# Performance work log

Hardware: AMD Instinct MI355X
Metric: run time of the kernel (lower is better)

The kernel has to match this reference:

```python
import jax, jax.numpy as jnp
import numpy as np

H = 256  # hidden_size
C = 512  # in_channels


def _gru_dir(x, w_ih, w_hh, b_ih, b_hh, reverse):
    # x: (B, T, Cin); w_ih: (3H, Cin); w_hh: (3H, H); gate order r,z,n (PyTorch)
    if reverse:
        x = x[:, ::-1, :]
    xp = jnp.einsum('btc,gc->btg', x, w_ih) + b_ih  # (B, T, 3H), batched GEMM
    h0 = jnp.zeros((x.shape[0], w_hh.shape[1]), x.dtype)

    def step(h, xp_t):  # xp_t: (B, 3H)
        gh = h @ w_hh.T + b_hh
        xr, xz, xn = jnp.split(xp_t, 3, axis=-1)
        hr, hz, hn = jnp.split(gh, 3, axis=-1)
        r = jax.nn.sigmoid(xr + hr)
        z = jax.nn.sigmoid(xz + hz)
        n = jnp.tanh(xn + r * hn)
        h_new = (1.0 - z) * n + z * h
        return h_new, h_new

    _, ys = jax.lax.scan(step, h0, jnp.swapaxes(xp, 0, 1))  # (T, B, H)
    ys = jnp.swapaxes(ys, 0, 1)  # (B, T, H)
    if reverse:
        ys = ys[:, ::-1, :]
    return ys


def _bigru_layer(x, wf, whf, bf, bhf, wr, whr, br, bhr):
    fwd = _gru_dir(x, wf, whf, bf, bhf, reverse=False)
    bwd = _gru_dir(x, wr, whr, br, bhr, reverse=True)
    return jnp.concatenate([fwd, bwd], axis=-1)  # (B, T, 2H)


def setup_inputs() -> dict:
    key = jax.random.key(0)
    ks = jax.random.split(key, 17)
    k = 1.0 / np.sqrt(H)  # PyTorch default init bound
    u = lambda kk, shp: jax.random.uniform(kk, shp, jnp.float32, -k, k)
    x = jax.random.normal(ks[0], (64, 512, 512, 1), jnp.float32)
    inp = {'x': x}
    # layer 0: input size C; layer 1: input size 2H
    sizes = {'l0': C, 'l1': 2 * H}
    i = 1
    for layer in ('l0', 'l1'):
        cin = sizes[layer]
        for d in ('f', 'r'):
            inp[f'w_ih_{layer}{d}'] = u(ks[i], (3 * H, cin)); i += 1
            inp[f'w_hh_{layer}{d}'] = u(ks[i], (3 * H, H)); i += 1
            inp[f'b_ih_{layer}{d}'] = u(ks[i], (3 * H,)); i += 1
            inp[f'b_hh_{layer}{d}'] = u(ks[i], (3 * H,)); i += 1
    return inp


def reference(x, w_ih_l0f, w_hh_l0f, b_ih_l0f, b_hh_l0f,
              w_ih_l0r, w_hh_l0r, b_ih_l0r, b_hh_l0r,
              w_ih_l1f, w_hh_l1f, b_ih_l1f, b_hh_l1f,
              w_ih_l1r, w_hh_l1r, b_ih_l1r, b_hh_l1r):
    b, c, w, h = x.shape
    seq = x.reshape(b, c, w * h).transpose(0, 2, 1)  # (B, T, C)
    y0 = _bigru_layer(seq, w_ih_l0f, w_hh_l0f, b_ih_l0f, b_hh_l0f,
                      w_ih_l0r, w_hh_l0r, b_ih_l0r, b_hh_l0r)
    y1 = _bigru_layer(y0, w_ih_l1f, w_hh_l1f, b_ih_l1f, b_hh_l1f,
                      w_ih_l1r, w_hh_l1r, b_ih_l1r, b_hh_l1r)
    return y1  # (B, T, 2H)
```

## Files before the change

kernel.cpp:

```cpp
#include <hip/hip_runtime.h>


typedef unsigned short u16;
typedef unsigned char u8;
typedef __attribute__((ext_vector_type(8))) short short8;
typedef __attribute__((ext_vector_type(4))) float f32x4;
typedef __attribute__((ext_vector_type(4))) int i32x4;

#define C1 (-1.4426950408889634f)
#define C2 (-2.8853900817779268f)
#define QS 258064.0f
#define C1S (C1 / QS)
#define C2S (C2 / QS)
#define MAGIC 12582912.0f

static __device__ __forceinline__ u16 f2bf(float x){
  union { float f; unsigned u; } v; v.f = x;
  unsigned r = v.u + 0x7fffu + ((v.u >> 16) & 1u);
  return (u16)(r >> 16);
}
static __device__ __forceinline__ float bf2f(u16 b){
  union { float f; unsigned u; } v; v.u = ((unsigned)b) << 16;
  return v.f;
}
static __device__ __forceinline__ unsigned cvt_pk_bf16(float lo, float hi){
  unsigned d;
  asm("v_cvt_pk_bf16_f32 %0, %1, %2" : "=v"(d) : "v"(lo), "v"(hi));
  return d;
}
static __device__ __forceinline__ unsigned q8(float x, float scale){
  union { float f; unsigned u; } v; v.f = fmaf(x, scale, MAGIC);
  return v.u & 0xffu;
}
#if __has_builtin(__builtin_amdgcn_exp2f)
#define EXP2(x) __builtin_amdgcn_exp2f(x)
#else
#define EXP2(x) exp2f(x)
#endif
#define RCP(x) __builtin_amdgcn_rcpf(x)
#define MFI8(a,b,c) __builtin_amdgcn_mfma_i32_16x16x64_i8((a),(b),(c),0,0,0)

#define TT 512
#define BB 64
#define HH 256
#define GG 768
#define CC 512

#define HLB 320

__global__ __launch_bounds__(256) void k_wconv(const float* __restrict__ wf,
    const float* __restrict__ wr, u16* __restrict__ Wb)
{
  const int idx = (blockIdx.x * 256 + threadIdx.x) * 4;
  const int half = GG * CC;
  const float* src = (idx < half) ? (wf + idx) : (wr + (idx - half));
  float4 v = *(const float4*)src;
  unsigned p0 = (unsigned)f2bf(v.x) | ((unsigned)f2bf(v.y) << 16);
  unsigned p1 = (unsigned)f2bf(v.z) | ((unsigned)f2bf(v.w) << 16);
  *(uint2*)&Wb[idx] = make_uint2(p0, p1);
}

__global__ __launch_bounds__(256) void k_transpose(const float* __restrict__ x,
                                                   u16* __restrict__ xT)
{
  __shared__ u16 tile[32][33];
  const int b  = blockIdx.z;
  const int c0 = blockIdx.y * 32, t0 = blockIdx.x * 32;
  const int tx = threadIdx.x & 31, ty = threadIdx.x >> 5;
  const float* xb = x + (size_t)b * CC * TT;
  #pragma unroll
  for (int i = 0; i < 4; ++i){
    int c = c0 + ty + i * 8;
    tile[ty + i * 8][tx] = f2bf(xb[(size_t)c * TT + t0 + tx]);
  }
  __syncthreads();
  const int bb2 = b >> 1, mrow = b & 1;
  #pragma unroll
  for (int i = 0; i < 4; ++i){
    int t = t0 + ty + i * 8;
    size_t rowp = ((size_t)bb2 * TT + t) * 2 + mrow;
    xT[rowp * CC + c0 + tx] = tile[tx][ty + i * 8];
  }
}

__global__ __launch_bounds__(256) void k_gemm(const u16* __restrict__ A,
    const u16* __restrict__ Wb,
    const float* __restrict__ bif, const float* __restrict__ bir,
    const float* __restrict__ bhf, const float* __restrict__ bhr,
    u16* __restrict__ xpA, u16* __restrict__ xpB)
{
  __shared__ u16 As[64][72];
  __shared__ u16 Bs[64][72];
  const int tid = threadIdx.x;
  const int n0  = blockIdx.x * 64;
  const int m0  = blockIdx.y * 64;
  const int dir = (n0 >= GG) ? 1 : 0;
  const int gb  = n0 - dir * GG;
  const float* BI = dir ? bir : bif;
  const float* BH = dir ? bhr : bhf;

  const int w = tid >> 6, l = tid & 63, q = l >> 4, r = l & 15;
  f32x4 acc[4] = {};

  for (int k0 = 0; k0 < CC; k0 += 64){
    #pragma unroll
    for (int i = 0; i < 2; ++i){
      int ch = tid + 256 * i;
      int row = ch >> 3, c8 = ch & 7;
      *(uint4*)&As[row][c8 * 8] =
          *(const uint4*)&A[(size_t)(m0 + row) * CC + k0 + c8 * 8];
      *(uint4*)&Bs[row][c8 * 8] =
          *(const uint4*)&Wb[(size_t)(n0 + row) * CC + k0 + c8 * 8];
    }
    __syncthreads();
    #pragma unroll
    for (int kk = 0; kk < 2; ++kk){
      short8 a = *(const short8*)&As[w * 16 + r][kk * 32 + q * 8];
      #pragma unroll
      for (int nt = 0; nt < 4; ++nt){
        short8 b = *(const short8*)&Bs[nt * 16 + r][kk * 32 + q * 8];
        acc[nt] = __builtin_amdgcn_mfma_f32_16x16x32_bf16(a, b, acc[nt], 0, 0, 0);
      }
    }
    __syncthreads();
  }
  #pragma unroll
  for (int nt = 0; nt < 4; ++nt){
    const int g  = gb + nt * 16 + r;
    const int gi = g >> 8;
    const int c  = g & 255;
    const int wvl = c >> 5, cw = c & 31;
    const int ct = cw >> 4, rp = cw & 15;
    const float bias = (gi < 2) ? (BI[g] + BH[g]) : BI[g];
    const float sc   = (gi < 2) ? C1 : C2;
    #pragma unroll
    for (int j = 0; j < 4; ++j){
      const int row  = m0 + w * 16 + q * 4 + j;
      const int t    = (row >> 1) & 511;
      const int bb2  = row >> 10;
      const int mrow = row & 1;
      const int lane = wvl * 64 + (ct * 2 + mrow) * 16 + rp;
      const size_t base = ((size_t)(dir * 32 + bb2) * TT + t) * 512 + lane;
      const u16 v = f2bf(sc * (acc[nt][j] + bias));
      if (gi < 2) xpA[base * 2 + gi] = v;
      else        xpB[base]          = v;
    }
  }
}

template<int OUT_F32>
__global__ __launch_bounds__(512, 2) void k_rec(
    const u16* __restrict__ xpA, const u16* __restrict__ xpB,
    const float* __restrict__ whf, const float* __restrict__ whr,
    const float* __restrict__ bhf, const float* __restrict__ bhr,
    void* __restrict__ yout)
{
  __shared__ __align__(16) u8 hl[2][2][HLB];
  const int tid = threadIdx.x;
  const int d = blockIdx.x >> 5, bb2 = blockIdx.x & 31;
  const int wv = tid >> 6, l = tid & 63, q = l >> 4, r = l & 15;
  const int upper = (l >= 32);
  const int rodd  = q & 1;
  const int rl = l & 1;
  const float* WH = d ? whr : whf;
  const float* BH = d ? bhr : bhf;

  i32x4 Bf[3][2][4];
  #pragma unroll
  for (int gi = 0; gi < 3; ++gi)
    #pragma unroll
    for (int ct = 0; ct < 2; ++ct){
      int g = gi * HH + wv * 32 + ct * 16 + r;
      #pragma unroll
      for (int kk = 0; kk < 4; ++kk){
        const float* s = &WH[(size_t)g * HH + kk * 64 + q * 16];
        i32x4 bfv;
        #pragma unroll
        for (int c4 = 0; c4 < 4; ++c4){
          float4 fv = *(const float4*)(s + c4 * 4);
          unsigned b0 = q8(fv.x, 2032.0f);
          unsigned b1 = q8(fv.y, 2032.0f);
          unsigned b2 = q8(fv.z, 2032.0f);
          unsigned b3 = q8(fv.w, 2032.0f);
          bfv[c4] = (int)(b0 | (b1 << 8) | (b2 << 16) | (b3 << 24));
        }
        Bf[gi][ct][kk] = bfv;
      }
    }

  const int col = wv * 32 + (upper ? 16 : 0) + r;
  const float bnl = C2 * BH[2 * HH + col];
  float ho = 0.0f;
  const i32x4 ZACC = {};

  for (int i = tid; i < 2 * 2 * HLB; i += 512) ((u8*)hl)[i] = 0;

  const int t0 = d ? (TT - 1) : 0;
  const int dstep = d ? -1 : 1;

  const size_t blk = (size_t)(d * 32 + bb2) * TT;
  const u16* pxA = xpA + ((blk + t0) * 512 + tid) * 2;
  const u16* pxB = xpB + ((blk + t0) * 512 + tid);
  const ptrdiff_t pxAs = (ptrdiff_t)dstep * 512 * 2;
  const ptrdiff_t pxBs = (ptrdiff_t)dstep * 512;

  struct XP { unsigned a; u16 b; };
  XP cxA, cxB;
  cxA.a = *(const unsigned*)pxA;  cxA.b = *pxB;
  pxA += pxAs; pxB += pxBs;

  u16*   py = nullptr;  float* pf = nullptr;
  if (OUT_F32){
    float* yf = (float*)yout;
    pf = yf + (((size_t)(bb2 * 2 + rodd) * TT + t0) * (2 * HH)) + (size_t)d * HH + col;
  } else {
    u16* yb = (u16*)yout;
    py = yb + (((size_t)bb2 * TT + t0) * 2 + rodd) * 512 + (size_t)d * HH + col;
  }
  const ptrdiff_t pys = (ptrdiff_t)dstep * 2 * 512;
  const ptrdiff_t pfs = (ptrdiff_t)dstep * 2 * HH;

  __syncthreads();

  auto step = [&](int s, int cur, XP* cxu, XP* cxl) {
    const int nxt = cur ^ 1;
    cxl->a = *(const unsigned*)pxA;
    cxl->b = *pxB;
    pxA += pxAs; pxB += pxBs;

    i32x4 af0 = *(const i32x4*)&hl[cur][rl][0 * 64 + q * 16];
    i32x4 af1 = *(const i32x4*)&hl[cur][rl][1 * 64 + q * 16];
    i32x4 af2 = *(const i32x4*)&hl[cur][rl][2 * 64 + q * 16];
    i32x4 af3 = *(const i32x4*)&hl[cur][rl][3 * 64 + q * 16];

    i32x4 a00 = MFI8(af0, Bf[0][0][0], ZACC);
    i32x4 a01 = MFI8(af0, Bf[0][1][0], ZACC);
    i32x4 a10 = MFI8(af0, Bf[1][0][0], ZACC);
    i32x4 a11 = MFI8(af0, Bf[1][1][0], ZACC);
    a00 = MFI8(af1, Bf[0][0][1], a00);  a01 = MFI8(af1, Bf[0][1][1], a01);
    a10 = MFI8(af1, Bf[1][0][1], a10);  a11 = MFI8(af1, Bf[1][1][1], a11);
    a00 = MFI8(af2, Bf[0][0][2], a00);  a01 = MFI8(af2, Bf[0][1][2], a01);
    a10 = MFI8(af2, Bf[1][0][2], a10);  a11 = MFI8(af2, Bf[1][1][2], a11);
    a00 = MFI8(af3, Bf[0][0][3], a00);  a01 = MFI8(af3, Bf[0][1][3], a01);
    a10 = MFI8(af3, Bf[1][0][3], a10);  a11 = MFI8(af3, Bf[1][1][3], a11);
    i32x4 a20 = MFI8(af0, Bf[2][0][0], ZACC);
    i32x4 a21 = MFI8(af0, Bf[2][1][0], ZACC);
    a20 = MFI8(af1, Bf[2][0][1], a20);  a21 = MFI8(af1, Bf[2][1][1], a21);
    a20 = MFI8(af2, Bf[2][0][2], a20);  a21 = MFI8(af2, Bf[2][1][2], a21);
    a20 = MFI8(af3, Bf[2][0][3], a20);  a21 = MFI8(af3, Bf[2][1][3], a21);

    int e00 = upper ? a01[0] : a00[0];
    int e01 = upper ? a01[1] : a00[1];
    int e10 = upper ? a11[0] : a10[0];
    int e11 = upper ? a11[1] : a10[1];
    float a0f = (float)(rodd ? e01 : e00);
    float a1f = (float)(rodd ? e11 : e10);
    float xrp = bf2f((u16)(cxu->a & 0xffffu));
    float xzp = bf2f((u16)(cxu->a >> 16));
    float er = EXP2(fmaf(a0f, C1S, xrp));
    float ez = EXP2(fmaf(a1f, C1S, xzp));
    float sr = 1.0f + er, sz = 1.0f + ez;
    float R  = RCP(sr * sz);
    float rr = sz * R;
    float zz = sr * R;
    int e20 = upper ? a21[0] : a20[0];
    int e21 = upper ? a21[1] : a20[1];
    float a2f = (float)(rodd ? e21 : e20);
    float xnp = bf2f(cxu->b);
    float inner = fmaf(a2f, C2S, bnl);
    float e2 = EXP2(fmaf(rr, inner, xnp));
    float nn = fmaf(2.0f, RCP(1.0f + e2), -1.0f);
    float hv = fmaf(zz, ho - nn, nn);
    ho = hv;
    hl[nxt][rodd][col] = (u8)q8(hv, 127.0f);
    if (OUT_F32){
      pf[0] = hv;
      pf += pfs;
    } else {
      py[0] = (u16)cvt_pk_bf16(hv, hv);
      py += pys;
    }
    asm volatile("s_waitcnt lgkmcnt(0)" ::: "memory");
    __builtin_amdgcn_s_barrier();
    asm volatile("" ::: "memory");
  };

  #pragma unroll 1
  for (int s = 0; s < TT; s += 2){
    step(s,     0, &cxA, &cxB);
    step(s + 1, 1, &cxB, &cxA);
  }
}

extern "C" void kernel_launch(void* const* d_in, const int* in_sizes, int n_in,
                              void* d_out, int out_size, void* d_ws, size_t ws_size,
                              hipStream_t stream)
{
  const float* x        = (const float*)d_in[0];
  const float* w_ih_l0f = (const float*)d_in[1];
  const float* w_hh_l0f = (const float*)d_in[2];
  const float* b_ih_l0f = (const float*)d_in[3];
  const float* b_hh_l0f = (const float*)d_in[4];
  const float* w_ih_l0r = (const float*)d_in[5];
  const float* w_hh_l0r = (const float*)d_in[6];
  const float* b_ih_l0r = (const float*)d_in[7];
  const float* b_hh_l0r = (const float*)d_in[8];
  const float* w_ih_l1f = (const float*)d_in[9];
  const float* w_hh_l1f = (const float*)d_in[10];
  const float* b_ih_l1f = (const float*)d_in[11];
  const float* b_hh_l1f = (const float*)d_in[12];
  const float* w_ih_l1r = (const float*)d_in[13];
  const float* w_hh_l1r = (const float*)d_in[14];
  const float* b_ih_l1r = (const float*)d_in[15];
  const float* b_hh_l1r = (const float*)d_in[16];

  u16* xT  = (u16*)d_ws;
  u16* xpA = xT  + (size_t)BB * TT * CC;
  u16* xpB = xpA + (size_t)64 * TT * 512 * 2;
  u16* Wb  = xpB + (size_t)64 * TT * 512;
  u16* y0  = xT;
  (void)in_sizes; (void)n_in; (void)out_size; (void)ws_size;

  k_transpose<<<dim3(TT / 32, CC / 32, BB), 256, 0, stream>>>(x, xT);

  k_wconv<<<dim3(2 * GG * CC / 1024), 256, 0, stream>>>(w_ih_l0f, w_ih_l0r, Wb);
  k_gemm<<<dim3(2 * GG / 64, BB * TT / 64), 256, 0, stream>>>(
      xT, Wb, b_ih_l0f, b_ih_l0r, b_hh_l0f, b_hh_l0r, xpA, xpB);

  k_rec<0><<<dim3(64), 512, 0, stream>>>(xpA, xpB, w_hh_l0f, w_hh_l0r, b_hh_l0f, b_hh_l0r, (void*)y0);

  k_wconv<<<dim3(2 * GG * CC / 1024), 256, 0, stream>>>(w_ih_l1f, w_ih_l1r, Wb);
  k_gemm<<<dim3(2 * GG / 64, BB * TT / 64), 256, 0, stream>>>(
      y0, Wb, b_ih_l1f, b_ih_l1r, b_hh_l1f, b_hh_l1r, xpA, xpB);

  k_rec<1><<<dim3(64), 512, 0, stream>>>(xpA, xpB, w_hh_l1f, w_hh_l1r, b_hh_l1f, b_hh_l1r, d_out);
}
```

Before: 849.2 us.

## Interleave two independent batch chains per recurrent block to hide latency

Each recurrent block now processes two batch groups (two independent recurrence chains) instead of one, halving the grid from 64 to 32 blocks. The MFMA and gate work of the two chains is interleaved inside each timestep so one chain's latency can overlap the other's, and the two chains share a single barrier per step. The cost is twice the serial per-step work per block, more registers and shared memory, and use of only half as many CUs on a latency-bound kernel.

```diff
diff --git a/kernel.cpp b/kernel.cpp
--- a/kernel.cpp
+++ b/kernel.cpp
@@ -155,9 +155,10 @@
     const float* __restrict__ bhf, const float* __restrict__ bhr,
     void* __restrict__ yout)
 {
-  __shared__ __align__(16) u8 hl[2][2][HLB];
+  __shared__ __align__(16) u8 hl[2][2][2][HLB];
   const int tid = threadIdx.x;
-  const int d = blockIdx.x >> 5, bb2 = blockIdx.x & 31;
+  const int d  = blockIdx.x >> 4;
+  const int qd = blockIdx.x & 15;
   const int wv = tid >> 6, l = tid & 63, q = l >> 4, r = l & 15;
   const int upper = (l >= 32);
   const int rodd  = q & 1;
@@ -190,73 +191,56 @@
 
   const int col = wv * 32 + (upper ? 16 : 0) + r;
   const float bnl = C2 * BH[2 * HH + col];
-  float ho = 0.0f;
+  float hoA = 0.0f, hoB = 0.0f;
   const i32x4 ZACC = {};
 
-  for (int i = tid; i < 2 * 2 * HLB; i += 512) ((u8*)hl)[i] = 0;
+  for (int i = tid; i < 2 * 2 * 2 * HLB; i += 512) ((u8*)hl)[i] = 0;
 
   const int t0 = d ? (TT - 1) : 0;
   const int dstep = d ? -1 : 1;
 
-  const size_t blk = (size_t)(d * 32 + bb2) * TT;
-  const u16* pxA = xpA + ((blk + t0) * 512 + tid) * 2;
-  const u16* pxB = xpB + ((blk + t0) * 512 + tid);
+  const int bbA = qd * 2;
+  const size_t blkA = (size_t)(d * 32 + bbA) * TT;
+  const u16* pxAA = xpA + ((blkA + t0) * 512 + tid) * 2;
+  const u16* pxBA = xpB + ((blkA + t0) * 512 + tid);
+  const u16* pxAB = pxAA + (size_t)TT * 512 * 2;
+  const u16* pxBB = pxBA + (size_t)TT * 512;
   const ptrdiff_t pxAs = (ptrdiff_t)dstep * 512 * 2;
   const ptrdiff_t pxBs = (ptrdiff_t)dstep * 512;
 
   struct XP { unsigned a; u16 b; };
-  XP cxA, cxB;
-  cxA.a = *(const unsigned*)pxA;  cxA.b = *pxB;
-  pxA += pxAs; pxB += pxBs;
-
-  u16*   py = nullptr;  float* pf = nullptr;
+  XP cA0, cA1, cB0, cB1;
+  cA0.a = *(const unsigned*)pxAA;  cA0.b = *pxBA;
+  cB0.a = *(const unsigned*)pxAB;  cB0.b = *pxBB;
+  pxAA += pxAs; pxBA += pxBs; pxAB += pxAs; pxBB += pxBs;
+
+  u16 *pyA = nullptr, *pyB = nullptr;
+  float *pfA = nullptr, *pfB = nullptr;
   if (OUT_F32){
     float* yf = (float*)yout;
-    pf = yf + (((size_t)(bb2 * 2 + rodd) * TT + t0) * (2 * HH)) + (size_t)d * HH + col;
+    pfA = yf + (((size_t)(bbA * 2 + rodd) * TT + t0) * (2 * HH)) + (size_t)d * HH + col;
+    pfB = pfA + (size_t)2 * TT * (2 * HH);
   } else {
     u16* yb = (u16*)yout;
-    py = yb + (((size_t)bb2 * TT + t0) * 2 + rodd) * 512 + (size_t)d * HH + col;
+    pyA = yb + (((size_t)bbA * TT + t0) * 2 + rodd) * 512 + (size_t)d * HH + col;
+    pyB = pyA + (size_t)TT * 2 * 512;
   }
   const ptrdiff_t pys = (ptrdiff_t)dstep * 2 * 512;
   const ptrdiff_t pfs = (ptrdiff_t)dstep * 2 * HH;
 
   __syncthreads();
 
-  auto step = [&](int s, int cur, XP* cxu, XP* cxl) {
-    const int nxt = cur ^ 1;
-    cxl->a = *(const unsigned*)pxA;
-    cxl->b = *pxB;
-    pxA += pxAs; pxB += pxBs;
-
-    i32x4 af0 = *(const i32x4*)&hl[cur][rl][0 * 64 + q * 16];
-    i32x4 af1 = *(const i32x4*)&hl[cur][rl][1 * 64 + q * 16];
-    i32x4 af2 = *(const i32x4*)&hl[cur][rl][2 * 64 + q * 16];
-    i32x4 af3 = *(const i32x4*)&hl[cur][rl][3 * 64 + q * 16];
-
-    i32x4 a00 = MFI8(af0, Bf[0][0][0], ZACC);
-    i32x4 a01 = MFI8(af0, Bf[0][1][0], ZACC);
-    i32x4 a10 = MFI8(af0, Bf[1][0][0], ZACC);
-    i32x4 a11 = MFI8(af0, Bf[1][1][0], ZACC);
-    a00 = MFI8(af1, Bf[0][0][1], a00);  a01 = MFI8(af1, Bf[0][1][1], a01);
-    a10 = MFI8(af1, Bf[1][0][1], a10);  a11 = MFI8(af1, Bf[1][1][1], a11);
-    a00 = MFI8(af2, Bf[0][0][2], a00);  a01 = MFI8(af2, Bf[0][1][2], a01);
-    a10 = MFI8(af2, Bf[1][0][2], a10);  a11 = MFI8(af2, Bf[1][1][2], a11);
-    a00 = MFI8(af3, Bf[0][0][3], a00);  a01 = MFI8(af3, Bf[0][1][3], a01);
-    a10 = MFI8(af3, Bf[1][0][3], a10);  a11 = MFI8(af3, Bf[1][1][3], a11);
-    i32x4 a20 = MFI8(af0, Bf[2][0][0], ZACC);
-    i32x4 a21 = MFI8(af0, Bf[2][1][0], ZACC);
-    a20 = MFI8(af1, Bf[2][0][1], a20);  a21 = MFI8(af1, Bf[2][1][1], a21);
-    a20 = MFI8(af2, Bf[2][0][2], a20);  a21 = MFI8(af2, Bf[2][1][2], a21);
-    a20 = MFI8(af3, Bf[2][0][3], a20);  a21 = MFI8(af3, Bf[2][1][3], a21);
-
+  auto gates = [&](const i32x4& a00, const i32x4& a01, const i32x4& a10,
+                   const i32x4& a11, const i32x4& a20, const i32x4& a21,
+                   unsigned xa, u16 xb, float& ho) -> float {
     int e00 = upper ? a01[0] : a00[0];
     int e01 = upper ? a01[1] : a00[1];
     int e10 = upper ? a11[0] : a10[0];
     int e11 = upper ? a11[1] : a10[1];
     float a0f = (float)(rodd ? e01 : e00);
     float a1f = (float)(rodd ? e11 : e10);
-    float xrp = bf2f((u16)(cxu->a & 0xffffu));
-    float xzp = bf2f((u16)(cxu->a >> 16));
+    float xrp = bf2f((u16)(xa & 0xffffu));
+    float xzp = bf2f((u16)(xa >> 16));
     float er = EXP2(fmaf(a0f, C1S, xrp));
     float ez = EXP2(fmaf(a1f, C1S, xzp));
     float sr = 1.0f + er, sz = 1.0f + ez;
@@ -266,19 +250,58 @@
     int e20 = upper ? a21[0] : a20[0];
     int e21 = upper ? a21[1] : a20[1];
     float a2f = (float)(rodd ? e21 : e20);
-    float xnp = bf2f(cxu->b);
+    float xnp = bf2f(xb);
     float inner = fmaf(a2f, C2S, bnl);
     float e2 = EXP2(fmaf(rr, inner, xnp));
     float nn = fmaf(2.0f, RCP(1.0f + e2), -1.0f);
     float hv = fmaf(zz, ho - nn, nn);
     ho = hv;
-    hl[nxt][rodd][col] = (u8)q8(hv, 127.0f);
+    return hv;
+  };
+
+  #define CHAIN_MFMA(CH, a00,a01,a10,a11,a20,a21)                              \
+    i32x4 af0 = *(const i32x4*)&hl[CH][cur][rl][0 * 64 + q * 16];              \
+    i32x4 af1 = *(const i32x4*)&hl[CH][cur][rl][1 * 64 + q * 16];              \
+    i32x4 af2 = *(const i32x4*)&hl[CH][cur][rl][2 * 64 + q * 16];              \
+    i32x4 af3 = *(const i32x4*)&hl[CH][cur][rl][3 * 64 + q * 16];              \
+    a00 = MFI8(af0, Bf[0][0][0], ZACC);                                        \
+    a01 = MFI8(af0, Bf[0][1][0], ZACC);                                        \
+    a10 = MFI8(af0, Bf[1][0][0], ZACC);                                        \
+    a11 = MFI8(af0, Bf[1][1][0], ZACC);                                        \
+    a00 = MFI8(af1, Bf[0][0][1], a00);  a01 = MFI8(af1, Bf[0][1][1], a01);     \
+    a10 = MFI8(af1, Bf[1][0][1], a10);  a11 = MFI8(af1, Bf[1][1][1], a11);     \
+    a00 = MFI8(af2, Bf[0][0][2], a00);  a01 = MFI8(af2, Bf[0][1][2], a01);     \
+    a10 = MFI8(af2, Bf[1][0][2], a10);  a11 = MFI8(af2, Bf[1][1][2], a11);     \
+    a00 = MFI8(af3, Bf[0][0][3], a00);  a01 = MFI8(af3, Bf[0][1][3], a01);     \
+    a10 = MFI8(af3, Bf[1][0][3], a10);  a11 = MFI8(af3, Bf[1][1][3], a11);     \
+    a20 = MFI8(af0, Bf[2][0][0], ZACC);                                        \
+    a21 = MFI8(af0, Bf[2][1][0], ZACC);                                        \
+    a20 = MFI8(af1, Bf[2][0][1], a20);  a21 = MFI8(af1, Bf[2][1][1], a21);     \
+    a20 = MFI8(af2, Bf[2][0][2], a20);  a21 = MFI8(af2, Bf[2][1][2], a21);     \
+    a20 = MFI8(af3, Bf[2][0][3], a20);  a21 = MFI8(af3, Bf[2][1][3], a21);
+
+  auto step = [&](int cur, XP* cAu, XP* cAl, XP* cBu, XP* cBl) {
+    const int nxt = cur ^ 1;
+    cAl->a = *(const unsigned*)pxAA;  cAl->b = *pxBA;
+    cBl->a = *(const unsigned*)pxAB;  cBl->b = *pxBB;
+    pxAA += pxAs; pxBA += pxBs; pxAB += pxAs; pxBB += pxBs;
+
+    i32x4 A00, A01, A10, A11, A20, A21;
+    { CHAIN_MFMA(0, A00, A01, A10, A11, A20, A21) }
+    i32x4 B00, B01, B10, B11, B20, B21;
+    { CHAIN_MFMA(1, B00, B01, B10, B11, B20, B21) }
+
+    float hvA = gates(A00, A01, A10, A11, A20, A21, cAu->a, cAu->b, hoA);
+    hl[0][nxt][rodd][col] = (u8)q8(hvA, 127.0f);
+    float hvB = gates(B00, B01, B10, B11, B20, B21, cBu->a, cBu->b, hoB);
+    hl[1][nxt][rodd][col] = (u8)q8(hvB, 127.0f);
     if (OUT_F32){
-      pf[0] = hv;
-      pf += pfs;
+      pfA[0] = hvA;  pfB[0] = hvB;
+      pfA += pfs;    pfB += pfs;
     } else {
-      py[0] = (u16)cvt_pk_bf16(hv, hv);
-      py += pys;
+      pyA[0] = (u16)cvt_pk_bf16(hvA, hvA);
+      pyB[0] = (u16)cvt_pk_bf16(hvB, hvB);
+      pyA += pys;    pyB += pys;
     }
     asm volatile("s_waitcnt lgkmcnt(0)" ::: "memory");
     __builtin_amdgcn_s_barrier();
@@ -287,9 +310,10 @@
 
   #pragma unroll 1
   for (int s = 0; s < TT; s += 2){
-    step(s,     0, &cxA, &cxB);
-    step(s + 1, 1, &cxB, &cxA);
-  }
+    step(0, &cA0, &cA1, &cB0, &cB1);
+    step(1, &cA1, &cA0, &cB1, &cB0);
+  }
+  #undef CHAIN_MFMA
 }
 
 extern "C" void kernel_launch(void* const* d_in, const int* in_sizes, int n_in,
@@ -327,11 +351,11 @@
   k_gemm<<<dim3(2 * GG / 64, BB * TT / 64), 256, 0, stream>>>(
       xT, Wb, b_ih_l0f, b_ih_l0r, b_hh_l0f, b_hh_l0r, xpA, xpB);
 
-  k_rec<0><<<dim3(64), 512, 0, stream>>>(xpA, xpB, w_hh_l0f, w_hh_l0r, b_hh_l0f, b_hh_l0r, (void*)y0);
+  k_rec<0><<<dim3(32), 512, 0, stream>>>(xpA, xpB, w_hh_l0f, w_hh_l0r, b_hh_l0f, b_hh_l0r, (void*)y0);
 
   k_wconv<<<dim3(2 * GG * CC / 1024), 256, 0, stream>>>(w_ih_l1f, w_ih_l1r, Wb);
   k_gemm<<<dim3(2 * GG / 64, BB * TT / 64), 256, 0, stream>>>(
       y0, Wb, b_ih_l1f, b_ih_l1r, b_hh_l1f, b_hh_l1r, xpA, xpB);
 
-  k_rec<1><<<dim3(64), 512, 0, stream>>>(xpA, xpB, w_hh_l1f, w_hh_l1r, b_hh_l1f, b_hh_l1r, d_out);
-}
+  k_rec<1><<<dim3(32), 512, 0, stream>>>(xpA, xpB, w_hh_l1f, w_hh_l1r, b_hh_l1f, b_hh_l1r, d_out);
+}
```

Result: slower. 1.263 ms (+48.8%).
